# Optimization experiments

Hardware: AMD Instinct MI355X
Metric: run time of the kernel (lower is better)

Reference implementation:

```python
import jax, jax.numpy as jnp
import numpy as np

L = 64      # lattice side
H = 32      # hiddenSize
D = 2       # inputDim (spin states)
B = 1024    # batch of configurations
LOG_PROB_FACTOR = 0.5


def setup_inputs() -> dict:
    key = jax.random.key(0)
    ks = jax.random.split(key, 6)
    s = 0.3  # uniform init half-width (mimics variance_scaling uniform)
    return {
        "x": jax.random.randint(ks[0], (B, L, L), 0, D, dtype=jnp.int32),
        "Win": jax.random.uniform(ks[1], (2 * D, H), minval=-s, maxval=s, dtype=jnp.float32),
        "WcH": jax.random.uniform(ks[2], (H, H), minval=-s, maxval=s, dtype=jnp.float32),
        "WcV": jax.random.uniform(ks[3], (H, H), minval=-s, maxval=s, dtype=jnp.float32),
        "bV": jnp.zeros((H,), dtype=jnp.float32),
        "Wout": jax.random.uniform(ks[4], (H, D), minval=-s, maxval=s, dtype=jnp.float32),
        "bout": (0.1 * jax.random.normal(ks[5], (D,))).astype(jnp.float32),
    }


def _rev(line, b, axis):
    # reverse_line: identity if direction b == 1 else flip along `axis`
    return jnp.where(b == 1, line, jnp.flip(line, axis=axis))


def reference(x, Win, WcH, WcV, bV, Wout, bout):
    Bn, Ln, _ = x.shape
    d = Wout.shape[1]
    h = WcH.shape[0]
    xoh = jax.nn.one_hot(x, d, dtype=Win.dtype)            # [B, L, L, d]
    direction = jnp.asarray(np.where(np.arange(Ln) % 2 == 0, 1, -1).astype(np.int32))

    def col_step(hcarry, cols):
        # hcarry: horizontal carry [B, h]; cols: (carryV [B,h], stateH [B,d], stateV [B,d])
        cV, sH, sV = cols
        newR = jnp.concatenate([sH, sV], axis=-1)          # [B, 2d]
        newC = jax.nn.elu(hcarry @ WcH + (cV @ WcV + bV) + newR @ Win)  # [B, h]
        out = newC @ Wout + bout                            # [B, d]
        return newC, (newC, jax.nn.log_softmax(out, axis=-1))

    def row_step(carry, inputs):
        carryV_grid, prevRow = carry                        # [B, L, h], [B, L, d]
        x_row, b = inputs                                   # [B, L, d], scalar direction
        cV_rev = _rev(carryV_grid, b, 1)
        x_rev = _rev(x_row, b, 1)
        prev_rev = _rev(prevRow, b, 1)
        # shifted previous-column state along scan direction
        stateH = jnp.concatenate(
            [jnp.zeros((Bn, 1, d), dtype=x_rev.dtype), x_rev], axis=1)[:, :-1]
        xs = (jnp.swapaxes(cV_rev, 0, 1),                   # [L, B, h]
              jnp.swapaxes(stateH, 0, 1),                   # [L, B, d]
              jnp.swapaxes(prev_rev, 0, 1))                 # [L, B, d]
        _, (carries, logsm) = jax.lax.scan(
            col_step, jnp.zeros((Bn, h), dtype=Win.dtype), xs)
        carries = jnp.swapaxes(carries, 0, 1)               # [B, L, h]
        logsm = jnp.swapaxes(logsm, 0, 1)                   # [B, L, d]
        logP = jnp.sum(_rev(logsm, b, 1) * x_row, axis=-1)  # [B, L]
        logP = jnp.nan_to_num(logP, nan=-35.0)
        return (_rev(carries, b, 1), x_row), logP

    init = (jnp.zeros((Bn, Ln, h), dtype=Win.dtype),
            jnp.zeros((Bn, Ln, d), dtype=Win.dtype))
    _, probs = jax.lax.scan(row_step, init, (jnp.moveaxis(xoh, 1, 0), direction))
    # probs: [L_rows, B, L_cols] -> per-sample log-prob
    return LOG_PROB_FACTOR * jnp.sum(probs, axis=(0, 2))   # [B]
```

## Files before the change

### kernel.cpp

```cpp
#include <hip/hip_runtime.h>
#include <cstdint>

namespace {

typedef _Float16 half_t;
typedef half_t half8  __attribute__((ext_vector_type(8)));
typedef __fp16 fp16x2 __attribute__((ext_vector_type(2)));
typedef float  f32x4  __attribute__((ext_vector_type(4)));

constexpr int LSIDE = 64;
constexpr int HID   = 32;
constexpr int NB    = 16;

__device__ __forceinline__ half8 as_h8(uint4 u) { return __builtin_bit_cast(half8, u); }
__device__ __forceinline__ uint4 as_u4(half8 h) { return __builtin_bit_cast(uint4, h); }
__device__ __forceinline__ unsigned pk2(float a, float b) {
    fp16x2 t = __builtin_amdgcn_cvt_pkrtz(a, b);
    return __builtin_bit_cast(unsigned, t);
}
__device__ __forceinline__ float elu1(float v) {
    float e = __expf(v) - 1.f;
    return v > 0.f ? v : e;
}
__device__ __forceinline__ half8 elupack(const f32x4& a1, const f32x4& a2) {
    uint4 nb;
    nb.x = pk2(elu1(a1[0]), elu1(a1[1]));
    nb.y = pk2(elu1(a1[2]), elu1(a1[3]));
    nb.z = pk2(elu1(a2[0]), elu1(a2[1]));
    nb.w = pk2(elu1(a2[2]), elu1(a2[3]));
    return as_h8(nb);
}

#define MFMA(a,b,c) __builtin_amdgcn_mfma_f32_16x16x32_f16((a),(b),(c),0,0,0)


__global__ __launch_bounds__(128) void rnn2d_pipe(
    const int*   __restrict__ x,
    const float* __restrict__ Win,
    const float* __restrict__ WcH,
    const float* __restrict__ WcV,
    const float* __restrict__ bV,
    const float* __restrict__ Wout,
    const float* __restrict__ bout,
    float*       __restrict__ out)
{
    const int tid = threadIdx.x;
    const int wv  = tid >> 6;
    const int l   = tid & 63;
    const int r_  = l & 15, g_ = l >> 4, n = l & 15;
    const int bbase = blockIdx.x * NB;

    __shared__ uint4 cvs[64 * 64];
    __shared__ f32x4 ringF[4 * 8 * 64 * 2];
    __shared__ unsigned sgnw[8 * 64];
    __shared__ float logpsh[64];

    for (int i = tid; i < 64 * 64; i += 128) cvs[i] = uint4{0u,0u,0u,0u};

    const int j1 = 8 * (r_ >> 2) + (r_ & 3), j2 = j1 + 4;
    half8 A1h, A2h, A1v, A2v, A3a, A3b, Awd;
#pragma unroll
    for (int e = 0; e < 8; ++e) {
        const int k = 8 * g_ + e;
        A1h[e] = (half_t)WcH[k * HID + j1];
        A2h[e] = (half_t)WcH[k * HID + j2];
        A1v[e] = (half_t)WcV[k * HID + j1];
        A2v[e] = (half_t)WcV[k * HID + j2];
        float a3a = 0.f, a3b = 0.f;
        if (k < 4)       { a3a = Win[k * HID + j1]; a3b = Win[k * HID + j2]; }
        else if (k == 4) { a3a = bV[j1];            a3b = bV[j2]; }
        A3a[e] = (half_t)a3a;
        A3b[e] = (half_t)a3b;
        Awd[e] = (half_t)((r_ == 0) ? (Wout[k * 2 + 1] - Wout[k * 2 + 0]) : 0.f);
    }
    const float db = bout[1] - bout[0];
    f32x4 dinit; dinit[0]=db; dinit[1]=db; dinit[2]=db; dinit[3]=db;
    f32x4 zc;    zc[0]=0.f;  zc[1]=0.f;  zc[2]=0.f;  zc[3]=0.f;
    const unsigned gm16 = (g_ == 0) ? 0x3C00u : 0u;

    const int* xw = x + (long)bbase * 4096;

    __syncthreads();

    unsigned long long rmc = 0ull, rm1 = 0ull;
    int xr[NB];
    float logp0 = 0.f, logp1 = 0.f;
    f32x4 Ua[4], Ub[4];
    half8 hc = as_h8(uint4{0u,0u,0u,0u});
    uint4 h7[8];
#pragma unroll
    for (int i = 0; i < 8; ++i) h7[i] = uint4{0u,0u,0u,0u};

    if (wv == 1) {
#pragma unroll
        for (int nn = 0; nn < NB; ++nn) xr[nn] = xw[nn * 4096 + l];
        {
            unsigned long long rm = 0ull;
#pragma unroll
            for (int nn = 0; nn < NB; ++nn) {
                unsigned long long bal = __ballot(xr[nn] == 1);
                rm = (n == nn) ? bal : rm;
            }
            rmc = rm;
        }
#pragma unroll
        for (int nn = 0; nn < NB; ++nn) xr[nn] = xw[nn * 4096 + 64 + l];

#pragma unroll
        for (int i = 0; i < 8; ++i) {
            unsigned aP = 0u;
            if (i > 0) {
                unsigned bl = (unsigned)((rmc >> (i - 1)) & 1ull);
                aP = gm16 << (bl << 4);
            }
            uint4 b3u{aP, 0u, gm16, 0u};
            f32x4 q1 = MFMA(A3a, as_h8(b3u), zc);
            f32x4 q2 = MFMA(A3b, as_h8(b3u), zc);
            ringF[((0*8 + i)*64 + l)*2 + 0] = q1;
            ringF[((0*8 + i)*64 + l)*2 + 1] = q2;
        }
#pragma unroll
        for (int i = 0; i < 8; ++i) {
            const int c = 8 + i;
            unsigned bl = (unsigned)((rmc >> (c - 1)) & 1ull);
            unsigned aP = gm16 << (bl << 4);
            uint4 b3u{aP, 0u, gm16, 0u};
            f32x4 q1 = MFMA(A3a, as_h8(b3u), zc);
            f32x4 q2 = MFMA(A3b, as_h8(b3u), zc);
            half8 cvh = as_h8(cvs[c*64 + l]);
            f32x4 p1 = MFMA(A1v, cvh, q1);
            f32x4 p2 = MFMA(A2v, cvh, q2);
            ringF[((1*8 + i)*64 + l)*2 + 0] = p1;
            ringF[((1*8 + i)*64 + l)*2 + 1] = p2;
        }
    }
    __syncthreads();

    if (wv == 0) {
        Ua[0] = ringF[((0*8+0)*64+l)*2+0]; Ub[0] = ringF[((0*8+0)*64+l)*2+1];
        Ua[1] = ringF[((0*8+1)*64+l)*2+0]; Ub[1] = ringF[((0*8+1)*64+l)*2+1];
        Ua[2] = ringF[((0*8+2)*64+l)*2+0]; Ub[2] = ringF[((0*8+2)*64+l)*2+1];
    }

    int c0 = 0, dir0 = 1;

#define PF(i)  { const int pf_=(i)+3; const int cs_=(gph+(pf_>>3))&3; const int ci_=pf_&7; \
                 Ua[((i)+3)&3] = ringF[((cs_*8+ci_)*64+l)*2+0];                            \
                 Ub[((i)+3)&3] = ringF[((cs_*8+ci_)*64+l)*2+1]; }

#define NORMAL(i) { PF(i)                                                                  \
      f32x4 a1 = MFMA(A1h, hc, Ua[(i)&3]); f32x4 a2 = MFMA(A2h, hc, Ub[(i)&3]);           \
      hc = elupack(a1, a2); cvs[c0*64+l] = as_u4(hc); c0 += dir0; }

#define NORM7(i) { PF(i)                                                                   \
      f32x4 a1 = MFMA(A1h, hc, Ua[(i)&3]); f32x4 a2 = MFMA(A2h, hc, Ub[(i)&3]);           \
      hc = elupack(a1, a2); cvs[c0*64+l] = as_u4(hc); h7[(i)] = as_u4(hc); c0 += dir0; }

#define SPECIAL(i) { PF(i)                                                                 \
      f32x4 pre1 = MFMA(A1v, as_h8(h7[7-(i)]), Ua[(i)&3]);                                 \
      f32x4 pre2 = MFMA(A2v, as_h8(h7[7-(i)]), Ub[(i)&3]);                                 \
      if (doOut) { f32x4 od = MFMA(Awd, as_h8(h7[7-(i)]), dinit);                          \
        float du = __int_as_float(__float_as_int(od[0]) ^ sgnw[(i)*64+l]);                 \
        logp0 -= __logf(1.f + __expf(du)); }                                               \
      f32x4 a1 = MFMA(A1h, hc, pre1); f32x4 a2 = MFMA(A2h, hc, pre2);                      \
      hc = elupack(a1, a2); cvs[c0*64+l] = as_u4(hc); c0 += dir0; }

    for (int gph = 0; gph < 512; ++gph) {
        const int k = gph & 7, rr = gph >> 3;
        if (wv == 0) {
            if (k == 0) {
                dir0 = (rr & 1) ? -1 : 1;
                c0   = (rr & 1) ? 63 : 0;
                hc   = as_h8(uint4{0u,0u,0u,0u});
                const bool doOut = (rr >= 1);
                SPECIAL(0) SPECIAL(1) SPECIAL(2) SPECIAL(3)
                SPECIAL(4) SPECIAL(5) SPECIAL(6) SPECIAL(7)
            } else if (k < 7) {
                NORMAL(0) NORMAL(1) NORMAL(2) NORMAL(3)
                NORMAL(4) NORMAL(5) NORMAL(6) NORMAL(7)
            } else {
                NORM7(0) NORM7(1) NORM7(2) NORM7(3)
                NORM7(4) NORM7(5) NORM7(6) NORM7(7)
            }
        } else {
            const int t = gph + 2;
            if (t < 512) {
                const int rp = t >> 3, kp = t & 7;
                const int dirp = (rp & 1) ? -1 : 1;
                if (kp == 0) {
                    rm1 = rmc;
                    {
                        unsigned long long rm = 0ull;
#pragma unroll
                        for (int nn = 0; nn < NB; ++nn) {
                            unsigned long long bal = __ballot(xr[nn] == 1);
                            rm = (n == nn) ? bal : rm;
                        }
                        rmc = rm;
                    }
                    const int nr = (rp < 63) ? rp + 1 : 63;
#pragma unroll
                    for (int nn = 0; nn < NB; ++nn) xr[nn] = xw[nn * 4096 + nr * 64 + l];
#pragma unroll
                    for (int i = 0; i < 8; ++i) {
                        const int c = (rp & 1) ? 63 - i : i;
                        unsigned aP = 0u;
                        if (i > 0) {
                            const int cl = c - dirp;
                            unsigned bl = (unsigned)((rmc >> cl) & 1ull);
                            aP = gm16 << (bl << 4);
                        }
                        unsigned bu = (unsigned)((rm1 >> c) & 1ull);
                        unsigned bP = gm16 << (bu << 4);
                        uint4 b3u{aP, bP, gm16, 0u};
                        f32x4 q1 = MFMA(A3a, as_h8(b3u), zc);
                        f32x4 q2 = MFMA(A3b, as_h8(b3u), zc);
                        const int slot = t & 3;
                        ringF[((slot*8 + i)*64 + l)*2 + 0] = q1;
                        ringF[((slot*8 + i)*64 + l)*2 + 1] = q2;
                        sgnw[i*64 + l] = bu << 31;
                    }
                } else {
                    const bool doOut = (rp >= 1);
#pragma unroll
                    for (int i = 0; i < 8; ++i) {
                        const int sg = 8 * kp + i;
                        const int c = (rp & 1) ? 63 - sg : sg;
                        half8 cvh = as_h8(cvs[c*64 + l]);
                        if (doOut) {
                            f32x4 od = MFMA(Awd, cvh, dinit);
                            unsigned s32 = (unsigned)((rm1 >> c) & 1ull) << 31;
                            float du = __int_as_float(__float_as_int(od[0]) ^ s32);
                            logp1 -= __logf(1.f + __expf(du));
                        }
                        const int cl = c - dirp;
                        unsigned bl = (unsigned)((rmc >> cl) & 1ull);
                        unsigned aP = gm16 << (bl << 4);
                        unsigned bP = 0u;
                        if (doOut) {
                            unsigned bu = (unsigned)((rm1 >> c) & 1ull);
                            bP = gm16 << (bu << 4);
                        }
                        uint4 b3u{aP, bP, gm16, 0u};
                        f32x4 q1 = MFMA(A3a, as_h8(b3u), zc);
                        f32x4 q2 = MFMA(A3b, as_h8(b3u), zc);
                        f32x4 p1 = MFMA(A1v, cvh, q1);
                        f32x4 p2 = MFMA(A2v, cvh, q2);
                        const int slot = t & 3;
                        ringF[((slot*8 + i)*64 + l)*2 + 0] = p1;
                        ringF[((slot*8 + i)*64 + l)*2 + 1] = p2;
                    }
                }
            }
        }
        __syncthreads();
    }

    if (wv == 0) logpsh[l] = logp0;
    __syncthreads();
    if (wv == 1) {
#pragma unroll 8
        for (int c = 0; c < 64; ++c) {
            half8 cvh = as_h8(cvs[c*64 + l]);
            f32x4 od = MFMA(Awd, cvh, dinit);
            unsigned s32 = (unsigned)((rmc >> c) & 1ull) << 31;
            float du = __int_as_float(__float_as_int(od[0]) ^ s32);
            logp1 -= __logf(1.f + __expf(du));
        }
        float tot = logp1 + logpsh[l];
        if (l < NB) out[bbase + n] = 0.5f * tot;
    }

#undef PF
#undef NORMAL
#undef NORM7
#undef SPECIAL
}

}

extern "C" void kernel_launch(void* const* d_in, const int* in_sizes, int n_in,
                              void* d_out, int out_size, void* d_ws, size_t ws_size,
                              hipStream_t stream) {
    (void)n_in; (void)out_size; (void)d_ws; (void)ws_size;
    const int*   x    = (const int*)  d_in[0];
    const float* Win  = (const float*)d_in[1];
    const float* WcH  = (const float*)d_in[2];
    const float* WcV  = (const float*)d_in[3];
    const float* bV   = (const float*)d_in[4];
    const float* Wout = (const float*)d_in[5];
    const float* bout = (const float*)d_in[6];
    float*       out  = (float*)d_out;

    const int B = in_sizes[0] / (LSIDE * LSIDE);
    rnn2d_pipe<<<B / NB, 128, 0, stream>>>(x, Win, WcH, WcV, bV, Wout, bout, out);
}
```

Before: 858.8 us.

## Add third wavefront to compute output log-probs off the critical path

Splits the per-block work across three wavefronts instead of two. The recurrence wave no longer computes output log-softmax terms in its special row-start phase, and the producer wave no longer computes them while building ring inputs. A new third wave reads the stored hidden states, including a buffered copy of the last 8 columns, and accumulates log-probabilities. The aim is to shorten the serial recurrence and producer paths. In exchange it adds a wave per block, more shared memory traffic and more barrier participants, and it also splits the ring into two arrays.

```diff
diff --git a/kernel.cpp b/kernel.cpp
--- a/kernel.cpp
+++ b/kernel.cpp
@@ -34,7 +34,7 @@
 #define MFMA(a,b,c) __builtin_amdgcn_mfma_f32_16x16x32_f16((a),(b),(c),0,0,0)
 
 
-__global__ __launch_bounds__(128) void rnn2d_pipe(
+__global__ __launch_bounds__(192) void rnn2d_pipe3(
     const int*   __restrict__ x,
     const float* __restrict__ Win,
     const float* __restrict__ WcH,
@@ -51,11 +51,11 @@
     const int bbase = blockIdx.x * NB;
 
     __shared__ uint4 cvs[64 * 64];
-    __shared__ f32x4 ringF[4 * 8 * 64 * 2];
-    __shared__ unsigned sgnw[8 * 64];
-    __shared__ float logpsh[64];
-
-    for (int i = tid; i < 64 * 64; i += 128) cvs[i] = uint4{0u,0u,0u,0u};
+    __shared__ f32x4 ring1[4 * 8 * 64];
+    __shared__ f32x4 ring2[4 * 8 * 64];
+    __shared__ uint4 h7buf[8 * 64];
+
+    for (int i = tid; i < 64 * 64; i += 192) cvs[i] = uint4{0u,0u,0u,0u};
 
     const int j1 = 8 * (r_ >> 2) + (r_ & 3), j2 = j1 + 4;
     half8 A1h, A2h, A1v, A2v, A3a, A3b, Awd;
@@ -84,14 +84,14 @@
 
     unsigned long long rmc = 0ull, rm1 = 0ull;
     int xr[NB];
-    float logp0 = 0.f, logp1 = 0.f;
+    float logp = 0.f;
     f32x4 Ua[4], Ub[4];
     half8 hc = as_h8(uint4{0u,0u,0u,0u});
     uint4 h7[8];
 #pragma unroll
     for (int i = 0; i < 8; ++i) h7[i] = uint4{0u,0u,0u,0u};
 
-    if (wv == 1) {
+    if (wv >= 1) {
 #pragma unroll
         for (int nn = 0; nn < NB; ++nn) xr[nn] = xw[nn * 4096 + l];
         {
@@ -105,7 +105,9 @@
         }
 #pragma unroll
         for (int nn = 0; nn < NB; ++nn) xr[nn] = xw[nn * 4096 + 64 + l];
-
+    }
+
+    if (wv == 1) {
 #pragma unroll
         for (int i = 0; i < 8; ++i) {
             unsigned aP = 0u;
@@ -114,10 +116,8 @@
                 aP = gm16 << (bl << 4);
             }
             uint4 b3u{aP, 0u, gm16, 0u};
-            f32x4 q1 = MFMA(A3a, as_h8(b3u), zc);
-            f32x4 q2 = MFMA(A3b, as_h8(b3u), zc);
-            ringF[((0*8 + i)*64 + l)*2 + 0] = q1;
-            ringF[((0*8 + i)*64 + l)*2 + 1] = q2;
+            ring1[(0*8 + i)*64 + l] = MFMA(A3a, as_h8(b3u), zc);
+            ring2[(0*8 + i)*64 + l] = MFMA(A3b, as_h8(b3u), zc);
         }
 #pragma unroll
         for (int i = 0; i < 8; ++i) {
@@ -125,28 +125,23 @@
             unsigned bl = (unsigned)((rmc >> (c - 1)) & 1ull);
             unsigned aP = gm16 << (bl << 4);
             uint4 b3u{aP, 0u, gm16, 0u};
-            f32x4 q1 = MFMA(A3a, as_h8(b3u), zc);
-            f32x4 q2 = MFMA(A3b, as_h8(b3u), zc);
-            half8 cvh = as_h8(cvs[c*64 + l]);
-            f32x4 p1 = MFMA(A1v, cvh, q1);
-            f32x4 p2 = MFMA(A2v, cvh, q2);
-            ringF[((1*8 + i)*64 + l)*2 + 0] = p1;
-            ringF[((1*8 + i)*64 + l)*2 + 1] = p2;
+            ring1[(1*8 + i)*64 + l] = MFMA(A3a, as_h8(b3u), zc);
+            ring2[(1*8 + i)*64 + l] = MFMA(A3b, as_h8(b3u), zc);
         }
     }
     __syncthreads();
 
     if (wv == 0) {
-        Ua[0] = ringF[((0*8+0)*64+l)*2+0]; Ub[0] = ringF[((0*8+0)*64+l)*2+1];
-        Ua[1] = ringF[((0*8+1)*64+l)*2+0]; Ub[1] = ringF[((0*8+1)*64+l)*2+1];
-        Ua[2] = ringF[((0*8+2)*64+l)*2+0]; Ub[2] = ringF[((0*8+2)*64+l)*2+1];
+        Ua[0] = ring1[0*64+l]; Ub[0] = ring2[0*64+l];
+        Ua[1] = ring1[1*64+l]; Ub[1] = ring2[1*64+l];
+        Ua[2] = ring1[2*64+l]; Ub[2] = ring2[2*64+l];
     }
 
     int c0 = 0, dir0 = 1;
 
 #define PF(i)  { const int pf_=(i)+3; const int cs_=(gph+(pf_>>3))&3; const int ci_=pf_&7; \
-                 Ua[((i)+3)&3] = ringF[((cs_*8+ci_)*64+l)*2+0];                            \
-                 Ub[((i)+3)&3] = ringF[((cs_*8+ci_)*64+l)*2+1]; }
+                 Ua[((i)+3)&3] = ring1[(cs_*8+ci_)*64+l];                                  \
+                 Ub[((i)+3)&3] = ring2[(cs_*8+ci_)*64+l]; }
 
 #define NORMAL(i) { PF(i)                                                                  \
       f32x4 a1 = MFMA(A1h, hc, Ua[(i)&3]); f32x4 a2 = MFMA(A2h, hc, Ub[(i)&3]);           \
@@ -154,25 +149,22 @@
 
 #define NORM7(i) { PF(i)                                                                   \
       f32x4 a1 = MFMA(A1h, hc, Ua[(i)&3]); f32x4 a2 = MFMA(A2h, hc, Ub[(i)&3]);           \
-      hc = elupack(a1, a2); cvs[c0*64+l] = as_u4(hc); h7[(i)] = as_u4(hc); c0 += dir0; }
+      hc = elupack(a1, a2); { uint4 u_ = as_u4(hc); cvs[c0*64+l] = u_; h7[(i)] = u_;      \
+      h7buf[(i)*64+l] = u_; } c0 += dir0; }
 
 #define SPECIAL(i) { PF(i)                                                                 \
-      f32x4 pre1 = MFMA(A1v, as_h8(h7[7-(i)]), Ua[(i)&3]);                                 \
-      f32x4 pre2 = MFMA(A2v, as_h8(h7[7-(i)]), Ub[(i)&3]);                                 \
-      if (doOut) { f32x4 od = MFMA(Awd, as_h8(h7[7-(i)]), dinit);                          \
-        float du = __int_as_float(__float_as_int(od[0]) ^ sgnw[(i)*64+l]);                 \
-        logp0 -= __logf(1.f + __expf(du)); }                                               \
-      f32x4 a1 = MFMA(A1h, hc, pre1); f32x4 a2 = MFMA(A2h, hc, pre2);                      \
+      f32x4 p1 = MFMA(A1v, as_h8(h7[7-(i)]), Ua[(i)&3]);                                   \
+      f32x4 p2 = MFMA(A2v, as_h8(h7[7-(i)]), Ub[(i)&3]);                                   \
+      f32x4 a1 = MFMA(A1h, hc, p1); f32x4 a2 = MFMA(A2h, hc, p2);                          \
       hc = elupack(a1, a2); cvs[c0*64+l] = as_u4(hc); c0 += dir0; }
 
     for (int gph = 0; gph < 512; ++gph) {
-        const int k = gph & 7, rr = gph >> 3;
         if (wv == 0) {
+            const int k = gph & 7, rr = gph >> 3;
             if (k == 0) {
                 dir0 = (rr & 1) ? -1 : 1;
                 c0   = (rr & 1) ? 63 : 0;
                 hc   = as_h8(uint4{0u,0u,0u,0u});
-                const bool doOut = (rr >= 1);
                 SPECIAL(0) SPECIAL(1) SPECIAL(2) SPECIAL(3)
                 SPECIAL(4) SPECIAL(5) SPECIAL(6) SPECIAL(7)
             } else if (k < 7) {
@@ -182,11 +174,65 @@
                 NORM7(0) NORM7(1) NORM7(2) NORM7(3)
                 NORM7(4) NORM7(5) NORM7(6) NORM7(7)
             }
+        } else if (wv == 1) {
+            const int t = gph + 2;
+            if (t < 512) {
+                const int rp = t >> 3, kp = t & 7;
+                const int dirp = (rp & 1) ? -1 : 1;
+                const int slot = t & 3;
+                if (kp == 0) {
+                    rm1 = rmc;
+                    {
+                        unsigned long long rm = 0ull;
+#pragma unroll
+                        for (int nn = 0; nn < NB; ++nn) {
+                            unsigned long long bal = __ballot(xr[nn] == 1);
+                            rm = (n == nn) ? bal : rm;
+                        }
+                        rmc = rm;
+                    }
+                    const int nr = (rp < 63) ? rp + 1 : 63;
+#pragma unroll
+                    for (int nn = 0; nn < NB; ++nn) xr[nn] = xw[nn * 4096 + nr * 64 + l];
+#pragma unroll
+                    for (int i = 0; i < 8; ++i) {
+                        const int c = (rp & 1) ? 63 - i : i;
+                        unsigned aP = 0u;
+                        if (i > 0) {
+                            unsigned bl = (unsigned)((rmc >> (c - dirp)) & 1ull);
+                            aP = gm16 << (bl << 4);
+                        }
+                        unsigned bu = (unsigned)((rm1 >> c) & 1ull);
+                        unsigned bP = gm16 << (bu << 4);
+                        uint4 b3u{aP, bP, gm16, 0u};
+                        ring1[(slot*8 + i)*64 + l] = MFMA(A3a, as_h8(b3u), zc);
+                        ring2[(slot*8 + i)*64 + l] = MFMA(A3b, as_h8(b3u), zc);
+                    }
+                } else {
+#pragma unroll
+                    for (int i = 0; i < 8; ++i) {
+                        const int sg = 8 * kp + i;
+                        const int c = (rp & 1) ? 63 - sg : sg;
+                        half8 cvh = as_h8(cvs[c*64 + l]);
+                        unsigned bl = (unsigned)((rmc >> (c - dirp)) & 1ull);
+                        unsigned aP = gm16 << (bl << 4);
+                        unsigned bP = 0u;
+                        if (rp >= 1) {
+                            unsigned bu = (unsigned)((rm1 >> c) & 1ull);
+                            bP = gm16 << (bu << 4);
+                        }
+                        uint4 b3u{aP, bP, gm16, 0u};
+                        f32x4 q1 = MFMA(A3a, as_h8(b3u), zc);
+                        f32x4 q2 = MFMA(A3b, as_h8(b3u), zc);
+                        ring1[(slot*8 + i)*64 + l] = MFMA(A1v, cvh, q1);
+                        ring2[(slot*8 + i)*64 + l] = MFMA(A2v, cvh, q2);
+                    }
+                }
+            }
         } else {
             const int t = gph + 2;
             if (t < 512) {
                 const int rp = t >> 3, kp = t & 7;
-                const int dirp = (rp & 1) ? -1 : 1;
                 if (kp == 0) {
                     rm1 = rmc;
                     {
@@ -201,54 +247,34 @@
                     const int nr = (rp < 63) ? rp + 1 : 63;
 #pragma unroll
                     for (int nn = 0; nn < NB; ++nn) xr[nn] = xw[nn * 4096 + nr * 64 + l];
-#pragma unroll
-                    for (int i = 0; i < 8; ++i) {
-                        const int c = (rp & 1) ? 63 - i : i;
-                        unsigned aP = 0u;
-                        if (i > 0) {
-                            const int cl = c - dirp;
-                            unsigned bl = (unsigned)((rmc >> cl) & 1ull);
-                            aP = gm16 << (bl << 4);
-                        }
-                        unsigned bu = (unsigned)((rm1 >> c) & 1ull);
-                        unsigned bP = gm16 << (bu << 4);
-                        uint4 b3u{aP, bP, gm16, 0u};
-                        f32x4 q1 = MFMA(A3a, as_h8(b3u), zc);
-                        f32x4 q2 = MFMA(A3b, as_h8(b3u), zc);
-                        const int slot = t & 3;
-                        ringF[((slot*8 + i)*64 + l)*2 + 0] = q1;
-                        ringF[((slot*8 + i)*64 + l)*2 + 1] = q2;
-                        sgnw[i*64 + l] = bu << 31;
-                    }
-                } else {
-                    const bool doOut = (rp >= 1);
+                } else if (rp >= 1) {
+                    f32x4 odv[8];
 #pragma unroll
                     for (int i = 0; i < 8; ++i) {
                         const int sg = 8 * kp + i;
                         const int c = (rp & 1) ? 63 - sg : sg;
-                        half8 cvh = as_h8(cvs[c*64 + l]);
-                        if (doOut) {
-                            f32x4 od = MFMA(Awd, cvh, dinit);
+                        odv[i] = MFMA(Awd, as_h8(cvs[c*64 + l]), dinit);
+                    }
+#pragma unroll
+                    for (int i = 0; i < 8; ++i) {
+                        const int sg = 8 * kp + i;
+                        const int c = (rp & 1) ? 63 - sg : sg;
+                        unsigned s32 = (unsigned)((rm1 >> c) & 1ull) << 31;
+                        float du = __int_as_float(__float_as_int(odv[i][0]) ^ s32);
+                        logp -= __logf(1.f + __expf(du));
+                    }
+                    if (kp == 2) {
+                        f32x4 odt[8];
+#pragma unroll
+                        for (int i = 0; i < 8; ++i)
+                            odt[i] = MFMA(Awd, as_h8(h7buf[i*64 + l]), dinit);
+#pragma unroll
+                        for (int i = 0; i < 8; ++i) {
+                            const int c = ((rp - 1) & 1) ? 7 - i : 56 + i;
                             unsigned s32 = (unsigned)((rm1 >> c) & 1ull) << 31;
-                            float du = __int_as_float(__float_as_int(od[0]) ^ s32);
-                            logp1 -= __logf(1.f + __expf(du));
-                        }
-                        const int cl = c - dirp;
-                        unsigned bl = (unsigned)((rmc >> cl) & 1ull);
-                        unsigned aP = gm16 << (bl << 4);
-                        unsigned bP = 0u;
-                        if (doOut) {
-                            unsigned bu = (unsigned)((rm1 >> c) & 1ull);
-                            bP = gm16 << (bu << 4);
-                        }
-                        uint4 b3u{aP, bP, gm16, 0u};
-                        f32x4 q1 = MFMA(A3a, as_h8(b3u), zc);
-                        f32x4 q2 = MFMA(A3b, as_h8(b3u), zc);
-                        f32x4 p1 = MFMA(A1v, cvh, q1);
-                        f32x4 p2 = MFMA(A2v, cvh, q2);
-                        const int slot = t & 3;
-                        ringF[((slot*8 + i)*64 + l)*2 + 0] = p1;
-                        ringF[((slot*8 + i)*64 + l)*2 + 1] = p2;
+                            float du = __int_as_float(__float_as_int(odt[i][0]) ^ s32);
+                            logp -= __logf(1.f + __expf(du));
+                        }
                     }
                 }
             }
@@ -256,19 +282,15 @@
         __syncthreads();
     }
 
-    if (wv == 0) logpsh[l] = logp0;
-    __syncthreads();
-    if (wv == 1) {
+    if (wv == 2) {
 #pragma unroll 8
         for (int c = 0; c < 64; ++c) {
-            half8 cvh = as_h8(cvs[c*64 + l]);
-            f32x4 od = MFMA(Awd, cvh, dinit);
+            f32x4 od = MFMA(Awd, as_h8(cvs[c*64 + l]), dinit);
             unsigned s32 = (unsigned)((rmc >> c) & 1ull) << 31;
             float du = __int_as_float(__float_as_int(od[0]) ^ s32);
-            logp1 -= __logf(1.f + __expf(du));
-        }
-        float tot = logp1 + logpsh[l];
-        if (l < NB) out[bbase + n] = 0.5f * tot;
+            logp -= __logf(1.f + __expf(du));
+        }
+        if (l < NB) out[bbase + n] = 0.5f * logp;
     }
 
 #undef PF
@@ -293,5 +315,5 @@
     float*       out  = (float*)d_out;
 
     const int B = in_sizes[0] / (LSIDE * LSIDE);
-    rnn2d_pipe<<<B / NB, 128, 0, stream>>>(x, Win, WcH, WcV, bV, Wout, bout, out);
-}
+    rnn2d_pipe3<<<B / NB, 192, 0, stream>>>(x, Win, WcH, WcV, bV, Wout, bout, out);
+}
```

Measured after the change: 789.7 us. -8.0%, faster.
